# Kernel tuning notes

Hardware: AMD Instinct MI355X
Metric: run time of the kernel (lower is better)

The kernel has to match this reference:

```python
import jax, jax.numpy as jnp
import numpy as np

B, S, DM = 2, 2048, 1024
H, HD = 16, 64          # n_heads, head_dim
TPF = 128               # tokens_per_frame
NF = S // TPF           # n_frames
EPS = 1e-6
ROPE_THETA = 10000.0
NEG = -1e30  # stand-in for -inf that stays finite under softmax


def setup_inputs() -> dict:
    key = jax.random.key(0)
    ks = jax.random.split(key, 3)
    x = jax.random.normal(ks[0], (B, S, DM), dtype=jnp.float32)
    Wqkv = jax.random.normal(ks[1], (3 * DM, DM), dtype=jnp.float32) * (DM ** -0.5)
    bqkv = jnp.zeros((3 * DM,), dtype=jnp.float32)
    Wout = jax.random.normal(ks[2], (DM, DM), dtype=jnp.float32) * (DM ** -0.5)
    bout = jnp.zeros((DM,), dtype=jnp.float32)
    q_scale = jnp.ones((HD,), dtype=jnp.float32)
    k_scale = jnp.ones((HD,), dtype=jnp.float32)
    return {"x": x, "Wqkv": Wqkv, "bqkv": bqkv, "q_scale": q_scale,
            "k_scale": k_scale, "Wout": Wout, "bout": bout}


def _block_causal_mask(dtype):
    # Frame-block causal: query in frame i may attend keys in frames <= i.
    # Quirk from source: rows of the LAST frame additionally mask frame 0.
    fr = jnp.arange(S) // TPF
    allowed = fr[None, :] <= fr[:, None]
    quirk = (fr[:, None] == NF - 1) & (fr[None, :] == 0)
    allowed = allowed & ~quirk
    return jnp.where(allowed, jnp.zeros((), dtype), jnp.full((), NEG, dtype))


def _rmsnorm(t, scale):
    return t * jax.lax.rsqrt(jnp.mean(t * t, axis=-1, keepdims=True) + EPS) * scale


def _rope(t):
    # half-split rotary over flat token index; t: [B,H,S,D]
    pos = jnp.arange(S, dtype=jnp.float32)
    inv_freq = 1.0 / (ROPE_THETA ** (jnp.arange(0, HD, 2, dtype=jnp.float32) / HD))
    ang = pos[:, None] * inv_freq[None, :]              # [S, D/2]
    cos = jnp.concatenate([jnp.cos(ang), jnp.cos(ang)], axis=-1)  # [S, D]
    sin = jnp.concatenate([jnp.sin(ang), jnp.sin(ang)], axis=-1)
    t1, t2 = jnp.split(t, 2, axis=-1)
    rot = jnp.concatenate([-t2, t1], axis=-1)
    return t * cos + rot * sin


def reference(x, Wqkv, bqkv, q_scale, k_scale, Wout, bout):
    qkv = x @ Wqkv.T + bqkv                        # [B,S,3*DM]
    qkv = qkv.reshape(B, S, 3, H, HD)
    q, k, v = jnp.moveaxis(qkv, 2, 0)              # each [B,S,H,D]
    q = jnp.transpose(q, (0, 2, 1, 3))             # [B,H,S,D]
    k = jnp.transpose(k, (0, 2, 1, 3))
    v = jnp.transpose(v, (0, 2, 1, 3))
    q = _rmsnorm(q, q_scale)
    k = _rmsnorm(k, k_scale)
    q = _rope(q)
    k = _rope(k)
    mask = _block_causal_mask(x.dtype)             # [S,S]
    scores = jnp.einsum('bhqd,bhkd->bhqk', q, k) * (HD ** -0.5) + mask
    attn = jax.nn.softmax(scores, axis=-1)
    o = jnp.einsum('bhqk,bhkd->bhqd', attn, v)     # [B,H,S,D]
    o = jnp.transpose(o, (0, 2, 1, 3)).reshape(B, S, DM)
    return o @ Wout.T + bout
```

## Files before the change

kernel.cpp:

```cpp
#include <hip/hip_runtime.h>
#include <cstddef>
#include <cstdint>

constexpr int CB  = 2;
constexpr int CS  = 2048;
constexpr int CDM = 1024;
constexpr int CH  = 16;
constexpr int CHD = 64;
constexpr int CTPF = 128;
constexpr int CNF = 16;

typedef __attribute__((ext_vector_type(8))) short short8;
typedef __attribute__((ext_vector_type(4))) float f32x4;

__device__ inline ushort f32_bf16_rne(float x) {
  uint32_t u = __float_as_uint(x);
  u += 0x7FFFu + ((u >> 16) & 1u);
  return (ushort)(u >> 16);
}
__device__ inline float bf16_f32(ushort h) {
  return __uint_as_float(((uint32_t)h) << 16);
}
__device__ inline void split8(const float* v, short8& H, short8& L) {
#pragma unroll
  for (int j = 0; j < 8; ++j) {
    const ushort hh = f32_bf16_rne(v[j]);
    H[j] = (short)hh;
    L[j] = (short)f32_bf16_rne(v[j] - bf16_f32(hh));
  }
}

__global__ __launch_bounds__(256) void rope_tab(float2* __restrict__ T) {
  const int idx = blockIdx.x * 256 + threadIdx.x;
  const int s = idx >> 5;
  const int j = idx & 31;
  const float inv = powf(10000.0f, -(float)j * (1.0f / 32.0f));
  const float ang = (float)s * inv;
  T[idx] = make_float2(cosf(ang), sinf(ang));
}

__global__ __launch_bounds__(256) void split3(
    const float* __restrict__ s0, ushort* __restrict__ h0,
    ushort* __restrict__ l0, int n0,
    const float* __restrict__ s1, ushort* __restrict__ h1,
    ushort* __restrict__ l1, int n1,
    const float* __restrict__ s2, ushort* __restrict__ h2,
    ushort* __restrict__ l2, int n2) {
  const int ntot = n0 + n1 + n2;
  int i = blockIdx.x * 256 + threadIdx.x;
  const int stride = gridDim.x * 256;
  for (; i < ntot; i += stride) {
    const float* src;
    ushort *h, *l;
    int j = i;
    if (j < n0) {
      src = s0; h = h0; l = l0;
    } else if ((j -= n0) < n1) {
      src = s1; h = h1; l = l1;
    } else {
      j -= n1; src = s2; h = h2; l = l2;
    }
    float v[8];
    *(float4*)&v[0] = ((const float4*)src)[2 * j];
    *(float4*)&v[4] = ((const float4*)src)[2 * j + 1];
    short8 H, L;
    split8(v, H, L);
    *(short8*)&h[(size_t)j * 8] = H;
    *(short8*)&l[(size_t)j * 8] = L;
  }
}

__global__ __launch_bounds__(256) void gemm_ps(
    const ushort* __restrict__ Ah, const ushort* __restrict__ Al,
    const ushort* __restrict__ Bh, const ushort* __restrict__ Bl,
    const float* __restrict__ bias, float* __restrict__ C,
    int M, int N, int K) {
  __shared__ ushort As_h[128 * 32], As_l[128 * 32];
  __shared__ ushort Bs_h[128 * 32], Bs_l[128 * 32];
  const int tid = threadIdx.x;
  const int bm = blockIdx.y * 128;
  const int bn = blockIdx.x * 128;
  const int wid = tid >> 6;
  const int lane = tid & 63;
  const int wm = wid >> 1;
  const int wn = wid & 1;
  const int l15 = lane & 15;
  const int lk = lane >> 4;
  const int srow = tid >> 2;
  const int kq = (tid & 3) * 8;

  f32x4 acc[4][4];
#pragma unroll
  for (int i = 0; i < 4; ++i)
#pragma unroll
    for (int j = 0; j < 4; ++j) acc[i][j] = (f32x4){0.f, 0.f, 0.f, 0.f};

  for (int k0 = 0; k0 < K; k0 += 32) {
    __syncthreads();
#pragma unroll
    for (int c = 0; c < 2; ++c) {
      const int row = srow + c * 64;
      const int kg = kq ^ ((row & 6) << 2);
      const size_t ga = (size_t)(bm + row) * K + k0 + kg;
      const size_t gb = (size_t)(bn + row) * K + k0 + kg;
      const int lo = tid * 8 + c * 2048;
      __builtin_amdgcn_global_load_lds(
          (const __attribute__((address_space(1))) void*)(Ah + ga),
          (__attribute__((address_space(3))) void*)&As_h[lo], 16, 0, 0);
      __builtin_amdgcn_global_load_lds(
          (const __attribute__((address_space(1))) void*)(Al + ga),
          (__attribute__((address_space(3))) void*)&As_l[lo], 16, 0, 0);
      __builtin_amdgcn_global_load_lds(
          (const __attribute__((address_space(1))) void*)(Bh + gb),
          (__attribute__((address_space(3))) void*)&Bs_h[lo], 16, 0, 0);
      __builtin_amdgcn_global_load_lds(
          (const __attribute__((address_space(1))) void*)(Bl + gb),
          (__attribute__((address_space(3))) void*)&Bs_l[lo], 16, 0, 0);
    }
    __syncthreads();

    short8 ah[4], al[4], bh[4], bl[4];
#pragma unroll
    for (int fI = 0; fI < 4; ++fI) {
      const int ar = wm * 64 + fI * 16 + l15;
      const int aoff = ar * 32 + ((lk * 8) ^ ((ar & 6) << 2));
      ah[fI] = *(const short8*)&As_h[aoff];
      al[fI] = *(const short8*)&As_l[aoff];
      const int br = wn * 64 + fI * 16 + l15;
      const int boff = br * 32 + ((lk * 8) ^ ((br & 6) << 2));
      bh[fI] = *(const short8*)&Bs_h[boff];
      bl[fI] = *(const short8*)&Bs_l[boff];
    }
#pragma unroll
    for (int mf = 0; mf < 4; ++mf)
#pragma unroll
      for (int nf = 0; nf < 4; ++nf) {
        acc[mf][nf] = __builtin_amdgcn_mfma_f32_16x16x32_bf16(
            ah[mf], bh[nf], acc[mf][nf], 0, 0, 0);
        acc[mf][nf] = __builtin_amdgcn_mfma_f32_16x16x32_bf16(
            ah[mf], bl[nf], acc[mf][nf], 0, 0, 0);
        acc[mf][nf] = __builtin_amdgcn_mfma_f32_16x16x32_bf16(
            al[mf], bh[nf], acc[mf][nf], 0, 0, 0);
      }
  }

#pragma unroll
  for (int mf = 0; mf < 4; ++mf)
#pragma unroll
    for (int nf = 0; nf < 4; ++nf) {
      const int col = bn + wn * 64 + nf * 16 + l15;
      const int row0 = bm + wm * 64 + mf * 16 + lk * 4;
      const float bc = bias[col];
#pragma unroll
      for (int i = 0; i < 4; ++i)
        C[(size_t)(row0 + i) * N + col] = acc[mf][nf][i] + bc;
    }
}

__global__ __launch_bounds__(256) void qkv_prep(
    const float* __restrict__ qkv, const float* __restrict__ q_scale,
    const float* __restrict__ k_scale, const float2* __restrict__ Trig,
    ushort* __restrict__ Qh, ushort* __restrict__ Ql,
    ushort* __restrict__ Kh, ushort* __restrict__ Kl,
    ushort* __restrict__ Vth, ushort* __restrict__ Vtl) {
  __shared__ float Vtile[64][68];
  const int lane = threadIdx.x & 63;
  const int w = threadIdx.x >> 6;
  const int st = blockIdx.x;
  const int h = blockIdx.y;
  const int b = blockIdx.z;

  const float qs = q_scale[lane];
  const float ks = k_scale[lane];
  const int j = lane & 31;
  const float sgn = (lane < 32) ? -1.f : 1.f;

  for (int it = 0; it < 16; ++it) {
    const int sl = w * 16 + it;
    const int s = st * 64 + sl;
    const size_t row =
        ((size_t)(b * CS + s)) * (3 * CDM) + (size_t)h * CHD + lane;
    float qv = qkv[row];
    float kv = qkv[row + CDM];
    const float vv = qkv[row + 2 * CDM];

    float sq = qv * qv, sk2 = kv * kv;
#pragma unroll
    for (int off = 32; off > 0; off >>= 1) {
      sq += __shfl_xor(sq, off);
      sk2 += __shfl_xor(sk2, off);
    }
    qv *= rsqrtf(sq * (1.f / CHD) + 1e-6f) * qs;
    kv *= rsqrtf(sk2 * (1.f / CHD) + 1e-6f) * ks;

    const float2 cstab = Trig[s * 32 + j];
    const float cs = cstab.x;
    const float sn = cstab.y;
    const float qp = __shfl_xor(qv, 32);
    const float kp = __shfl_xor(kv, 32);
    const float qr = fmaf(qv, cs, sgn * qp * sn) * 0.125f;
    const float kr = fmaf(kv, cs, sgn * kp * sn);

    const size_t tok = ((size_t)(b * CH + h)) * CS + s;
    const size_t obq = tok * CHD + lane;
    const ushort qhh = f32_bf16_rne(qr);
    Qh[obq] = qhh;
    Ql[obq] = f32_bf16_rne(qr - bf16_f32(qhh));
    const size_t obk = tok * CHD + (lane ^ ((s & 7) << 3));
    const ushort khh = f32_bf16_rne(kr);
    Kh[obk] = khh;
    Kl[obk] = f32_bf16_rne(kr - bf16_f32(khh));
    Vtile[lane][sl] = vv;
  }
  __syncthreads();
  const int d = threadIdx.x >> 2;
  const int sq4 = (threadIdx.x & 3) * 16;
  const size_t vrow = (((size_t)(b * CH + h)) * CHD + d) * CS + st * 64;
  const int vmk = (d & 7) << 3;
#pragma unroll
  for (int j0 = 0; j0 < 16; j0 += 8) {
    float v8[8];
#pragma unroll
    for (int jj = 0; jj < 8; ++jj) v8[jj] = Vtile[d][sq4 + j0 + jj];
    short8 H, L;
    split8(v8, H, L);
    const int c0 = (sq4 + j0) ^ vmk;
    *(short8*)&Vth[vrow + c0] = H;
    *(short8*)&Vtl[vrow + c0] = L;
  }
}

__global__ __launch_bounds__(256, 2) void attn_fwd_mfma(
    const ushort* __restrict__ Qh, const ushort* __restrict__ Ql,
    const ushort* __restrict__ Kh, const ushort* __restrict__ Kl,
    const ushort* __restrict__ Vth, const ushort* __restrict__ Vtl,
    ushort* __restrict__ Oh, ushort* __restrict__ Ol) {
  __shared__ ushort Ks_h[64 * 64], Ks_l[64 * 64];
  __shared__ ushort Vs_h[64 * 64], Vs_l[64 * 64];
  __shared__ ushort Ps_h[128 * 64], Ps_l[128 * 64];
  const int tid = threadIdx.x;
  const int b = blockIdx.x;
  const int h = blockIdx.y;
  const int fsel = blockIdx.z;
  const int f = (fsel < 8) ? (15 - fsel) : (fsel - 8);
  const int lane = tid & 63;
  const int wid = tid >> 6;
  const int l15 = lane & 15;
  const int lk = lane >> 4;
  const int qb = wid * 32;
  const size_t hb = ((size_t)(b * CH + h)) * CS * CHD;
  const size_t vtb = ((size_t)(b * CH + h)) * CHD * CS;

  short8 qh[2][2], ql[2][2];
#pragma unroll
  for (int nf = 0; nf < 2; ++nf)
#pragma unroll
    for (int ks = 0; ks < 2; ++ks) {
      const size_t qoff = hb +
          (size_t)(f * CTPF + qb + nf * 16 + l15) * CHD + ks * 32 + lk * 8;
      qh[nf][ks] = *(const short8*)(Qh + qoff);
      ql[nf][ks] = *(const short8*)(Ql + qoff);
    }

  f32x4 accO[2][4];
#pragma unroll
  for (int mo = 0; mo < 2; ++mo)
#pragma unroll
    for (int no = 0; no < 4; ++no) accO[mo][no] = (f32x4){0.f, 0.f, 0.f, 0.f};
  float m[2] = {-1e30f, -1e30f};
  float lsum[2] = {0.f, 0.f};

  const int kf0 = (f == CNF - 1) ? 1 : 0;
  for (int kf = kf0; kf <= f; ++kf) {
#pragma unroll 1
    for (int half = 0; half < 2; ++half) {
      const int cb = kf * CTPF + half * 64;
      __syncthreads();
      {
        const size_t kc = hb + (size_t)cb * CHD;
#pragma unroll
        for (int q = 0; q < 2; ++q) {
          const int u = tid * 8 + q * 2048;
          __builtin_amdgcn_global_load_lds(
              (const __attribute__((address_space(1))) void*)(Kh + kc + u),
              (__attribute__((address_space(3))) void*)&Ks_h[u], 16, 0, 0);
          __builtin_amdgcn_global_load_lds(
              (const __attribute__((address_space(1))) void*)(Kl + kc + u),
              (__attribute__((address_space(3))) void*)&Ks_l[u], 16, 0, 0);
          const size_t va = vtb + (size_t)(u >> 6) * CS + cb + (u & 63);
          __builtin_amdgcn_global_load_lds(
              (const __attribute__((address_space(1))) void*)(Vth + va),
              (__attribute__((address_space(3))) void*)&Vs_h[u], 16, 0, 0);
          __builtin_amdgcn_global_load_lds(
              (const __attribute__((address_space(1))) void*)(Vtl + va),
              (__attribute__((address_space(3))) void*)&Vs_l[u], 16, 0, 0);
        }
      }
      __syncthreads();

      f32x4 sacc[4][2];
#pragma unroll
      for (int mf = 0; mf < 4; ++mf)
#pragma unroll
        for (int nf = 0; nf < 2; ++nf) sacc[mf][nf] = (f32x4){0.f, 0.f, 0.f, 0.f};
#pragma unroll
      for (int ks = 0; ks < 2; ++ks) {
        short8 kh[4], kl[4];
#pragma unroll
        for (int mf = 0; mf < 4; ++mf) {
          const int krow = mf * 16 + l15;
          const int base = krow * 64 + ((ks * 32 + lk * 8) ^ ((krow & 7) << 3));
          kh[mf] = *(const short8*)&Ks_h[base];
          kl[mf] = *(const short8*)&Ks_l[base];
        }
#pragma unroll
        for (int mf = 0; mf < 4; ++mf)
#pragma unroll
          for (int nf = 0; nf < 2; ++nf) {
            sacc[mf][nf] = __builtin_amdgcn_mfma_f32_16x16x32_bf16(
                kh[mf], qh[nf][ks], sacc[mf][nf], 0, 0, 0);
            sacc[mf][nf] = __builtin_amdgcn_mfma_f32_16x16x32_bf16(
                kh[mf], ql[nf][ks], sacc[mf][nf], 0, 0, 0);
            sacc[mf][nf] = __builtin_amdgcn_mfma_f32_16x16x32_bf16(
                kl[mf], qh[nf][ks], sacc[mf][nf], 0, 0, 0);
          }
      }

      float c[2];
#pragma unroll
      for (int nf = 0; nf < 2; ++nf) {
        float cm = sacc[0][nf][0];
#pragma unroll
        for (int mf = 0; mf < 4; ++mf)
#pragma unroll
          for (int i = 0; i < 4; ++i) cm = fmaxf(cm, sacc[mf][nf][i]);
        cm = fmaxf(cm, __shfl_xor(cm, 16));
        cm = fmaxf(cm, __shfl_xor(cm, 32));
        const float mn = fmaxf(m[nf], cm);
        c[nf] = __expf(m[nf] - mn);
        m[nf] = mn;
        float ps = 0.f;
        const int qrow = qb + nf * 16 + l15;
        const int qmk = (qrow & 7) << 3;
#pragma unroll
        for (int mf = 0; mf < 4; ++mf) {
          float p0 = __expf(sacc[mf][nf][0] - mn);
          float p1 = __expf(sacc[mf][nf][1] - mn);
          float p2 = __expf(sacc[mf][nf][2] - mn);
          float p3 = __expf(sacc[mf][nf][3] - mn);
          ps += (p0 + p1) + (p2 + p3);
          const ushort h0 = f32_bf16_rne(p0), h1 = f32_bf16_rne(p1);
          const ushort h2 = f32_bf16_rne(p2), h3 = f32_bf16_rne(p3);
          uint2 hw, lw;
          hw.x = (uint32_t)h0 | ((uint32_t)h1 << 16);
          hw.y = (uint32_t)h2 | ((uint32_t)h3 << 16);
          lw.x = (uint32_t)f32_bf16_rne(p0 - bf16_f32(h0)) |
                 ((uint32_t)f32_bf16_rne(p1 - bf16_f32(h1)) << 16);
          lw.y = (uint32_t)f32_bf16_rne(p2 - bf16_f32(h2)) |
                 ((uint32_t)f32_bf16_rne(p3 - bf16_f32(h3)) << 16);
          const int off = qrow * 64 + ((mf * 16 + lk * 4) ^ qmk);
          *(uint2*)&Ps_h[off] = hw;
          *(uint2*)&Ps_l[off] = lw;
        }
        ps += __shfl_xor(ps, 16);
        ps += __shfl_xor(ps, 32);
        lsum[nf] = lsum[nf] * c[nf] + ps;
      }
#pragma unroll
      for (int mo = 0; mo < 2; ++mo)
#pragma unroll
        for (int i = 0; i < 4; ++i) {
          const float cq = __shfl(c[mo], lk * 4 + i);
#pragma unroll
          for (int no = 0; no < 4; ++no) accO[mo][no][i] *= cq;
        }

#pragma unroll
      for (int ks = 0; ks < 2; ++ks) {
        short8 pa_h[2], pa_l[2], vb_h[4], vb_l[4];
#pragma unroll
        for (int mo = 0; mo < 2; ++mo) {
          const int qrow = qb + mo * 16 + l15;
          const int base = qrow * 64 + ((ks * 32 + lk * 8) ^ ((qrow & 7) << 3));
          pa_h[mo] = *(const short8*)&Ps_h[base];
          pa_l[mo] = *(const short8*)&Ps_l[base];
        }
#pragma unroll
        for (int no = 0; no < 4; ++no) {
          const int vrow = no * 16 + l15;
          const int base = vrow * 64 + ((ks * 32 + lk * 8) ^ ((vrow & 7) << 3));
          vb_h[no] = *(const short8*)&Vs_h[base];
          vb_l[no] = *(const short8*)&Vs_l[base];
        }
#pragma unroll
        for (int mo = 0; mo < 2; ++mo)
#pragma unroll
          for (int no = 0; no < 4; ++no) {
            accO[mo][no] = __builtin_amdgcn_mfma_f32_16x16x32_bf16(
                pa_h[mo], vb_h[no], accO[mo][no], 0, 0, 0);
            accO[mo][no] = __builtin_amdgcn_mfma_f32_16x16x32_bf16(
                pa_h[mo], vb_l[no], accO[mo][no], 0, 0, 0);
            accO[mo][no] = __builtin_amdgcn_mfma_f32_16x16x32_bf16(
                pa_l[mo], vb_h[no], accO[mo][no], 0, 0, 0);
          }
      }
    }
  }

  const float il0 = 1.f / lsum[0];
  const float il1 = 1.f / lsum[1];
#pragma unroll
  for (int mo = 0; mo < 2; ++mo) {
    const float myil = (mo == 0) ? il0 : il1;
#pragma unroll
    for (int i = 0; i < 4; ++i) {
      const float wv = __shfl(myil, lk * 4 + i);
      const int srow = f * CTPF + qb + mo * 16 + lk * 4 + i;
      const size_t obase = (size_t)(b * CS + srow) * CDM + h * CHD;
#pragma unroll
      for (int no = 0; no < 4; ++no) {
        const float val = accO[mo][no][i] * wv;
        const ushort hh = f32_bf16_rne(val);
        Oh[obase + no * 16 + l15] = hh;
        Ol[obase + no * 16 + l15] = f32_bf16_rne(val - bf16_f32(hh));
      }
    }
  }
}

extern "C" void kernel_launch(void* const* d_in, const int* in_sizes, int n_in,
                              void* d_out, int out_size, void* d_ws, size_t ws_size,
                              hipStream_t stream) {
  const float* x       = (const float*)d_in[0];
  const float* Wqkv    = (const float*)d_in[1];
  const float* bqkv    = (const float*)d_in[2];
  const float* q_scale = (const float*)d_in[3];
  const float* k_scale = (const float*)d_in[4];
  const float* Wout    = (const float*)d_in[5];
  const float* bout    = (const float*)d_in[6];
  float* out = (float*)d_out;

  ushort* W = (ushort*)d_ws;
  const size_t qkvN = (size_t)(CB * CS) * (3 * CDM);
  const size_t perA = (size_t)CB * CH * CS * CHD;
  const size_t WqN  = (size_t)(3 * CDM) * CDM;
  const size_t WoN  = (size_t)CDM * CDM;

  float*  qkvF = (float*)W;
  ushort* Oh   = W;
  ushort* Ol   = W + perA;
  ushort* R1   = W + 2 * qkvN;
  ushort* Qh = R1;            ushort* Ql = R1 + perA;
  ushort* Kh = R1 + 2 * perA; ushort* Kl = R1 + 3 * perA;
  ushort* Vth = R1 + 4 * perA; ushort* Vtl = R1 + 5 * perA;
  ushort* xh  = R1;            ushort* xl  = R1 + perA;
  ushort* Wqh = R1 + 2 * perA; ushort* Wql = Wqh + WqN;
  ushort* Wouth = R1 + 6 * perA; ushort* Woutl = Wouth + WoN;
  float2* Trig = (float2*)(Woutl + WoN);

  rope_tab<<<256, 256, 0, stream>>>(Trig);
  split3<<<2048, 256, 0, stream>>>(x, xh, xl, (int)(perA / 8),
                                   Wqkv, Wqh, Wql, (int)(WqN / 8),
                                   Wout, Wouth, Woutl, (int)(WoN / 8));

  dim3 g1((3 * CDM) / 128, (CB * CS) / 128);
  gemm_ps<<<g1, 256, 0, stream>>>(xh, xl, Wqh, Wql, bqkv, qkvF,
                                  CB * CS, 3 * CDM, CDM);

  dim3 g2(CS / 64, CH, CB);
  qkv_prep<<<g2, 256, 0, stream>>>(qkvF, q_scale, k_scale, Trig,
                                   Qh, Ql, Kh, Kl, Vth, Vtl);

  dim3 g3(CB, CH, CNF);
  attn_fwd_mfma<<<g3, 256, 0, stream>>>(Qh, Ql, Kh, Kl, Vth, Vtl, Oh, Ol);

  dim3 g4(CDM / 128, (CB * CS) / 128);
  gemm_ps<<<g4, 256, 0, stream>>>(Oh, Ol, Wouth, Woutl, bout, out,
                                  CB * CS, CDM, CDM);
}
```

Baseline: 254.1 us.

## Split attention block across 8 waves with 16 query rows each

```diff
diff --git a/kernel.cpp b/kernel.cpp
--- a/kernel.cpp
+++ b/kernel.cpp
@@ -230,7 +230,7 @@
   }
 }
 
-__global__ __launch_bounds__(256, 2) void attn_fwd_mfma(
+__global__ __launch_bounds__(512, 4) void attn_fwd_mfma(
     const ushort* __restrict__ Qh, const ushort* __restrict__ Ql,
     const ushort* __restrict__ Kh, const ushort* __restrict__ Kl,
     const ushort* __restrict__ Vth, const ushort* __restrict__ Vtl,
@@ -247,28 +247,24 @@
   const int wid = tid >> 6;
   const int l15 = lane & 15;
   const int lk = lane >> 4;
-  const int qb = wid * 32;
+  const int qb = wid * 16;
   const size_t hb = ((size_t)(b * CH + h)) * CS * CHD;
   const size_t vtb = ((size_t)(b * CH + h)) * CHD * CS;
 
-  short8 qh[2][2], ql[2][2];
-#pragma unroll
-  for (int nf = 0; nf < 2; ++nf)
-#pragma unroll
-    for (int ks = 0; ks < 2; ++ks) {
-      const size_t qoff = hb +
-          (size_t)(f * CTPF + qb + nf * 16 + l15) * CHD + ks * 32 + lk * 8;
-      qh[nf][ks] = *(const short8*)(Qh + qoff);
-      ql[nf][ks] = *(const short8*)(Ql + qoff);
-    }
-
-  f32x4 accO[2][4];
-#pragma unroll
-  for (int mo = 0; mo < 2; ++mo)
-#pragma unroll
-    for (int no = 0; no < 4; ++no) accO[mo][no] = (f32x4){0.f, 0.f, 0.f, 0.f};
-  float m[2] = {-1e30f, -1e30f};
-  float lsum[2] = {0.f, 0.f};
+  short8 qh[2], ql[2];
+#pragma unroll
+  for (int ks = 0; ks < 2; ++ks) {
+    const size_t qoff = hb +
+        (size_t)(f * CTPF + qb + l15) * CHD + ks * 32 + lk * 8;
+    qh[ks] = *(const short8*)(Qh + qoff);
+    ql[ks] = *(const short8*)(Ql + qoff);
+  }
+
+  f32x4 accO[4];
+#pragma unroll
+  for (int no = 0; no < 4; ++no) accO[no] = (f32x4){0.f, 0.f, 0.f, 0.f};
+  float m = -1e30f;
+  float lsum = 0.f;
 
   const int kf0 = (f == CNF - 1) ? 1 : 0;
   for (int kf = kf0; kf <= f; ++kf) {
@@ -278,31 +274,26 @@
       __syncthreads();
       {
         const size_t kc = hb + (size_t)cb * CHD;
-#pragma unroll
-        for (int q = 0; q < 2; ++q) {
-          const int u = tid * 8 + q * 2048;
-          __builtin_amdgcn_global_load_lds(
-              (const __attribute__((address_space(1))) void*)(Kh + kc + u),
-              (__attribute__((address_space(3))) void*)&Ks_h[u], 16, 0, 0);
-          __builtin_amdgcn_global_load_lds(
-              (const __attribute__((address_space(1))) void*)(Kl + kc + u),
-              (__attribute__((address_space(3))) void*)&Ks_l[u], 16, 0, 0);
-          const size_t va = vtb + (size_t)(u >> 6) * CS + cb + (u & 63);
-          __builtin_amdgcn_global_load_lds(
-              (const __attribute__((address_space(1))) void*)(Vth + va),
-              (__attribute__((address_space(3))) void*)&Vs_h[u], 16, 0, 0);
-          __builtin_amdgcn_global_load_lds(
-              (const __attribute__((address_space(1))) void*)(Vtl + va),
-              (__attribute__((address_space(3))) void*)&Vs_l[u], 16, 0, 0);
-        }
+        const int u = tid * 8;
+        __builtin_amdgcn_global_load_lds(
+            (const __attribute__((address_space(1))) void*)(Kh + kc + u),
+            (__attribute__((address_space(3))) void*)&Ks_h[u], 16, 0, 0);
+        __builtin_amdgcn_global_load_lds(
+            (const __attribute__((address_space(1))) void*)(Kl + kc + u),
+            (__attribute__((address_space(3))) void*)&Ks_l[u], 16, 0, 0);
+        const size_t va = vtb + (size_t)(u >> 6) * CS + cb + (u & 63);
+        __builtin_amdgcn_global_load_lds(
+            (const __attribute__((address_space(1))) void*)(Vth + va),
+            (__attribute__((address_space(3))) void*)&Vs_h[u], 16, 0, 0);
+        __builtin_amdgcn_global_load_lds(
+            (const __attribute__((address_space(1))) void*)(Vtl + va),
+            (__attribute__((address_space(3))) void*)&Vs_l[u], 16, 0, 0);
       }
       __syncthreads();
 
-      f32x4 sacc[4][2];
-#pragma unroll
-      for (int mf = 0; mf < 4; ++mf)
-#pragma unroll
-        for (int nf = 0; nf < 2; ++nf) sacc[mf][nf] = (f32x4){0.f, 0.f, 0.f, 0.f};
+      f32x4 sacc[4];
+#pragma unroll
+      for (int mf = 0; mf < 4; ++mf) sacc[mf] = (f32x4){0.f, 0.f, 0.f, 0.f};
 #pragma unroll
       for (int ks = 0; ks < 2; ++ks) {
         short8 kh[4], kl[4];
@@ -314,77 +305,67 @@
           kl[mf] = *(const short8*)&Ks_l[base];
         }
 #pragma unroll
-        for (int mf = 0; mf < 4; ++mf)
-#pragma unroll
-          for (int nf = 0; nf < 2; ++nf) {
-            sacc[mf][nf] = __builtin_amdgcn_mfma_f32_16x16x32_bf16(
-                kh[mf], qh[nf][ks], sacc[mf][nf], 0, 0, 0);
-            sacc[mf][nf] = __builtin_amdgcn_mfma_f32_16x16x32_bf16(
-                kh[mf], ql[nf][ks], sacc[mf][nf], 0, 0, 0);
-            sacc[mf][nf] = __builtin_amdgcn_mfma_f32_16x16x32_bf16(
-                kl[mf], qh[nf][ks], sacc[mf][nf], 0, 0, 0);
-          }
-      }
-
-      float c[2];
-#pragma unroll
-      for (int nf = 0; nf < 2; ++nf) {
-        float cm = sacc[0][nf][0];
-#pragma unroll
-        for (int mf = 0; mf < 4; ++mf)
-#pragma unroll
-          for (int i = 0; i < 4; ++i) cm = fmaxf(cm, sacc[mf][nf][i]);
-        cm = fmaxf(cm, __shfl_xor(cm, 16));
-        cm = fmaxf(cm, __shfl_xor(cm, 32));
-        const float mn = fmaxf(m[nf], cm);
-        c[nf] = __expf(m[nf] - mn);
-        m[nf] = mn;
-        float ps = 0.f;
-        const int qrow = qb + nf * 16 + l15;
-        const int qmk = (qrow & 7) << 3;
-#pragma unroll
         for (int mf = 0; mf < 4; ++mf) {
-          float p0 = __expf(sacc[mf][nf][0] - mn);
-          float p1 = __expf(sacc[mf][nf][1] - mn);
-          float p2 = __expf(sacc[mf][nf][2] - mn);
-          float p3 = __expf(sacc[mf][nf][3] - mn);
-          ps += (p0 + p1) + (p2 + p3);
-          const ushort h0 = f32_bf16_rne(p0), h1 = f32_bf16_rne(p1);
-          const ushort h2 = f32_bf16_rne(p2), h3 = f32_bf16_rne(p3);
-          uint2 hw, lw;
-          hw.x = (uint32_t)h0 | ((uint32_t)h1 << 16);
-          hw.y = (uint32_t)h2 | ((uint32_t)h3 << 16);
-          lw.x = (uint32_t)f32_bf16_rne(p0 - bf16_f32(h0)) |
-                 ((uint32_t)f32_bf16_rne(p1 - bf16_f32(h1)) << 16);
-          lw.y = (uint32_t)f32_bf16_rne(p2 - bf16_f32(h2)) |
-                 ((uint32_t)f32_bf16_rne(p3 - bf16_f32(h3)) << 16);
-          const int off = qrow * 64 + ((mf * 16 + lk * 4) ^ qmk);
-          *(uint2*)&Ps_h[off] = hw;
-          *(uint2*)&Ps_l[off] = lw;
+          sacc[mf] = __builtin_amdgcn_mfma_f32_16x16x32_bf16(
+              kh[mf], qh[ks], sacc[mf], 0, 0, 0);
+          sacc[mf] = __builtin_amdgcn_mfma_f32_16x16x32_bf16(
+              kh[mf], ql[ks], sacc[mf], 0, 0, 0);
+          sacc[mf] = __builtin_amdgcn_mfma_f32_16x16x32_bf16(
+              kl[mf], qh[ks], sacc[mf], 0, 0, 0);
         }
-        ps += __shfl_xor(ps, 16);
-        ps += __shfl_xor(ps, 32);
-        lsum[nf] = lsum[nf] * c[nf] + ps;
-      }
-#pragma unroll
-      for (int mo = 0; mo < 2; ++mo)
-#pragma unroll
-        for (int i = 0; i < 4; ++i) {
-          const float cq = __shfl(c[mo], lk * 4 + i);
-#pragma unroll
-          for (int no = 0; no < 4; ++no) accO[mo][no][i] *= cq;
-        }
+      }
+
+      float cm = sacc[0][0];
+#pragma unroll
+      for (int mf = 0; mf < 4; ++mf)
+#pragma unroll
+        for (int i = 0; i < 4; ++i) cm = fmaxf(cm, sacc[mf][i]);
+      cm = fmaxf(cm, __shfl_xor(cm, 16));
+      cm = fmaxf(cm, __shfl_xor(cm, 32));
+      const float mn = fmaxf(m, cm);
+      const float c = __expf(m - mn);
+      m = mn;
+      float ps = 0.f;
+      const int qrow = qb + l15;
+      const int qmk = (qrow & 7) << 3;
+#pragma unroll
+      for (int mf = 0; mf < 4; ++mf) {
+        float p0 = __expf(sacc[mf][0] - mn);
+        float p1 = __expf(sacc[mf][1] - mn);
+        float p2 = __expf(sacc[mf][2] - mn);
+        float p3 = __expf(sacc[mf][3] - mn);
+        ps += (p0 + p1) + (p2 + p3);
+        const ushort h0 = f32_bf16_rne(p0), h1 = f32_bf16_rne(p1);
+        const ushort h2 = f32_bf16_rne(p2), h3 = f32_bf16_rne(p3);
+        uint2 hw, lw;
+        hw.x = (uint32_t)h0 | ((uint32_t)h1 << 16);
+        hw.y = (uint32_t)h2 | ((uint32_t)h3 << 16);
+        lw.x = (uint32_t)f32_bf16_rne(p0 - bf16_f32(h0)) |
+               ((uint32_t)f32_bf16_rne(p1 - bf16_f32(h1)) << 16);
+        lw.y = (uint32_t)f32_bf16_rne(p2 - bf16_f32(h2)) |
+               ((uint32_t)f32_bf16_rne(p3 - bf16_f32(h3)) << 16);
+        const int off = qrow * 64 + ((mf * 16 + lk * 4) ^ qmk);
+        *(uint2*)&Ps_h[off] = hw;
+        *(uint2*)&Ps_l[off] = lw;
+      }
+      ps += __shfl_xor(ps, 16);
+      ps += __shfl_xor(ps, 32);
+      lsum = lsum * c + ps;
+
+#pragma unroll
+      for (int i = 0; i < 4; ++i) {
+        const float cq = __shfl(c, lk * 4 + i);
+#pragma unroll
+        for (int no = 0; no < 4; ++no) accO[no][i] *= cq;
+      }
 
 #pragma unroll
       for (int ks = 0; ks < 2; ++ks) {
-        short8 pa_h[2], pa_l[2], vb_h[4], vb_l[4];
-#pragma unroll
-        for (int mo = 0; mo < 2; ++mo) {
-          const int qrow = qb + mo * 16 + l15;
-          const int base = qrow * 64 + ((ks * 32 + lk * 8) ^ ((qrow & 7) << 3));
-          pa_h[mo] = *(const short8*)&Ps_h[base];
-          pa_l[mo] = *(const short8*)&Ps_l[base];
-        }
+        const int prow = qb + l15;
+        const int pbase = prow * 64 + ((ks * 32 + lk * 8) ^ ((prow & 7) << 3));
+        const short8 pa_h = *(const short8*)&Ps_h[pbase];
+        const short8 pa_l = *(const short8*)&Ps_l[pbase];
+        short8 vb_h[4], vb_l[4];
 #pragma unroll
         for (int no = 0; no < 4; ++no) {
           const int vrow = no * 16 + l15;
@@ -393,37 +374,30 @@
           vb_l[no] = *(const short8*)&Vs_l[base];
         }
 #pragma unroll
-        for (int mo = 0; mo < 2; ++mo)
-#pragma unroll
-          for (int no = 0; no < 4; ++no) {
-            accO[mo][no] = __builtin_amdgcn_mfma_f32_16x16x32_bf16(
-                pa_h[mo], vb_h[no], accO[mo][no], 0, 0, 0);
-            accO[mo][no] = __builtin_amdgcn_mfma_f32_16x16x32_bf16(
-                pa_h[mo], vb_l[no], accO[mo][no], 0, 0, 0);
-            accO[mo][no] = __builtin_amdgcn_mfma_f32_16x16x32_bf16(
-                pa_l[mo], vb_h[no], accO[mo][no], 0, 0, 0);
-          }
-      }
-    }
-  }
-
-  const float il0 = 1.f / lsum[0];
-  const float il1 = 1.f / lsum[1];
-#pragma unroll
-  for (int mo = 0; mo < 2; ++mo) {
-    const float myil = (mo == 0) ? il0 : il1;
-#pragma unroll
-    for (int i = 0; i < 4; ++i) {
-      const float wv = __shfl(myil, lk * 4 + i);
-      const int srow = f * CTPF + qb + mo * 16 + lk * 4 + i;
-      const size_t obase = (size_t)(b * CS + srow) * CDM + h * CHD;
-#pragma unroll
-      for (int no = 0; no < 4; ++no) {
-        const float val = accO[mo][no][i] * wv;
-        const ushort hh = f32_bf16_rne(val);
-        Oh[obase + no * 16 + l15] = hh;
-        Ol[obase + no * 16 + l15] = f32_bf16_rne(val - bf16_f32(hh));
-      }
+        for (int no = 0; no < 4; ++no) {
+          accO[no] = __builtin_amdgcn_mfma_f32_16x16x32_bf16(
+              pa_h, vb_h[no], accO[no], 0, 0, 0);
+          accO[no] = __builtin_amdgcn_mfma_f32_16x16x32_bf16(
+              pa_h, vb_l[no], accO[no], 0, 0, 0);
+          accO[no] = __builtin_amdgcn_mfma_f32_16x16x32_bf16(
+              pa_l, vb_h[no], accO[no], 0, 0, 0);
+        }
+      }
+    }
+  }
+
+  const float il = 1.f / lsum;
+#pragma unroll
+  for (int i = 0; i < 4; ++i) {
+    const float wv = __shfl(il, lk * 4 + i);
+    const int srow = f * CTPF + qb + lk * 4 + i;
+    const size_t obase = (size_t)(b * CS + srow) * CDM + h * CHD;
+#pragma unroll
+    for (int no = 0; no < 4; ++no) {
+      const float val = accO[no][i] * wv;
+      const ushort hh = f32_bf16_rne(val);
+      Oh[obase + no * 16 + l15] = hh;
+      Ol[obase + no * 16 + l15] = f32_bf16_rne(val - bf16_f32(hh));
     }
   }
 }
@@ -472,7 +446,7 @@
                                    Qh, Ql, Kh, Kl, Vth, Vtl);
 
   dim3 g3(CB, CH, CNF);
-  attn_fwd_mfma<<<g3, 256, 0, stream>>>(Qh, Ql, Kh, Kl, Vth, Vtl, Oh, Ol);
+  attn_fwd_mfma<<<g3, 512, 0, stream>>>(Qh, Ql, Kh, Kl, Vth, Vtl, Oh, Ol);
 
   dim3 g4(CDM / 128, (CB * CS) / 128);
   gemm_ps<<<g4, 256, 0, stream>>>(Oh, Ol, Wouth, Woutl, bout, out,
```

After: 246.6 us (median of 2 runs). -3.0%, faster.
